# Kernel tuning notes

Hardware: AMD Instinct MI355X
Metric: run time of the kernel (lower is better)

## Reference

```python
import jax, jax.numpy as jnp
from jax import lax
import numpy as np

KSIZE = 5  # kernel_size from init
CHANNEL = 256

def _gaussian_kernel2d(sigma, ksize):
    # matches torch: exp(-i^2/(2*sigma^2)) outer product, normalized to sum 1
    n = ksize // 2
    r = jnp.arange(-n, n + 1, dtype=jnp.float32)
    g = jnp.exp(-(r ** 2) / (2.0 * sigma ** 2))
    k2d = g[:, None] * g[None, :]
    return k2d / k2d.sum()

def setup_inputs() -> dict:
    key = jax.random.key(0)
    k1, k2 = jax.random.split(key)
    x = jax.random.normal(k1, (16, CHANNEL, 64, 64), dtype=jnp.float32)
    # sigma is the module's learned scalar; keep away from 0 for a well-defined kernel
    sigma = jax.random.uniform(k2, (1,), dtype=jnp.float32, minval=0.5, maxval=1.5)
    return {"x": x, "sigma": sigma}

def reference(x, sigma):
    # The torch module writes a channel-diagonal weight into a dense Conv2d;
    # mathematically this is a depthwise conv with the same 2D Gaussian per channel.
    C = x.shape[1]
    k2d = _gaussian_kernel2d(sigma[0], KSIZE)
    w = jnp.broadcast_to(k2d[None, None, :, :], (C, 1, KSIZE, KSIZE))  # OIHW, groups=C
    pad = KSIZE // 2
    return lax.conv_general_dilated(
        x, w,
        window_strides=(1, 1),
        padding=[(pad, pad), (pad, pad)],
        dimension_numbers=("NCHW", "OIHW", "NCHW"),
        feature_group_count=C,
    )
```

## Files before the change

### kernel.cpp

```cpp
#include <hip/hip_runtime.h>
#include <math.h>


constexpr int Hh   = 64;
constexpr int Ww   = 64;
constexpr int KS   = 5;
constexpr int PADc = 2;
constexpr int TH   = Hh + 2 * PADc;
constexpr int IN_STR = 72;

__global__ __launch_bounds__(256, 6) void gauss5(const float* __restrict__ x,
                                                 const float* __restrict__ sigma,
                                                 float* __restrict__ out) {
    __shared__ float sIn[TH * IN_STR];

    const int t = threadIdx.x;
    const size_t plane = blockIdx.x;
    const float* __restrict__ xp = x + plane * (size_t)(Hh * Ww);
    float* __restrict__ op = out + plane * (size_t)(Hh * Ww);

    const float sg = sigma[0];
    const float c2 = -1.0f / (2.0f * sg * sg);
    float g[KS];
    float gsum = 0.0f;
#pragma unroll
    for (int i = 0; i < KS; ++i) {
        float d = (float)(i - PADc);
        g[i] = expf(d * d * c2);
        gsum += g[i];
    }
    const float ginv = 1.0f / gsum;
#pragma unroll
    for (int i = 0; i < KS; ++i) g[i] *= ginv;

    for (int i = t; i < 528; i += 256) {
        if (i < 272) {
            int rr  = i / 68;
            int cc  = i - rr * 68;
            int row = (rr < 2) ? rr : (rr + 64);
            sIn[row * IN_STR + cc] = 0.0f;
        } else {
            int j   = i - 272;
            int row = 2 + (j >> 2);
            int k   = j & 3;
            int col = (k < 2) ? k : (k + 64);
            sIn[row * IN_STR + col] = 0.0f;
        }
    }

    const float4* __restrict__ x4 = (const float4*)xp;
#pragma unroll
    for (int k = 0; k < 4; ++k) {
        int idx = t + k * 256;
        int r   = idx >> 4;
        int c   = (idx & 15) << 2;
        float4 v = x4[idx];
        float* dst = &sIn[(r + PADc) * IN_STR + c + PADc];
        dst[0] = v.x; dst[1] = v.y; dst[2] = v.z; dst[3] = v.w;
    }
    __syncthreads();

    const int c4 = t & 15;
    const int r0 = (t >> 4) << 2;

    float4 h[8];
#pragma unroll
    for (int i = 0; i < 8; ++i) {
        const float* src = &sIn[(r0 + i) * IN_STR + (c4 << 2)];
        float4 a = *(const float4*)(src);
        float4 b = *(const float4*)(src + 4);
        h[i].x = g[0]*a.x + g[1]*a.y + g[2]*a.z + g[3]*a.w + g[4]*b.x;
        h[i].y = g[0]*a.y + g[1]*a.z + g[2]*a.w + g[3]*b.x + g[4]*b.y;
        h[i].z = g[0]*a.z + g[1]*a.w + g[2]*b.x + g[3]*b.y + g[4]*b.z;
        h[i].w = g[0]*a.w + g[1]*b.x + g[2]*b.y + g[3]*b.z + g[4]*b.w;
    }

    float4* __restrict__ o4 = (float4*)op;
#pragma unroll
    for (int i = 0; i < 4; ++i) {
        float4 acc;
        acc.x = g[0]*h[i].x; acc.y = g[0]*h[i].y;
        acc.z = g[0]*h[i].z; acc.w = g[0]*h[i].w;
#pragma unroll
        for (int j = 1; j < KS; ++j) {
            acc.x += g[j] * h[i+j].x;
            acc.y += g[j] * h[i+j].y;
            acc.z += g[j] * h[i+j].z;
            acc.w += g[j] * h[i+j].w;
        }
        o4[(r0 + i) * 16 + c4] = acc;
    }
}

extern "C" void kernel_launch(void* const* d_in, const int* in_sizes, int n_in,
                              void* d_out, int out_size, void* d_ws, size_t ws_size,
                              hipStream_t stream) {
    const float* x     = (const float*)d_in[0];
    const float* sigma = (const float*)d_in[1];
    float* out         = (float*)d_out;
    const int planes = in_sizes[0] / (Hh * Ww);
    gauss5<<<planes, 256, 0, stream>>>(x, sigma, out);
}
```

Before: 118.7 us.

## Process four planes per block with double-buffered LDS and register prefetch

```diff
diff --git a/kernel.cpp b/kernel.cpp
--- a/kernel.cpp
+++ b/kernel.cpp
@@ -8,16 +8,15 @@
 constexpr int PADc = 2;
 constexpr int TH   = Hh + 2 * PADc;
 constexpr int IN_STR = 72;
+constexpr int PPB  = 4;
 
-__global__ __launch_bounds__(256, 6) void gauss5(const float* __restrict__ x,
+__global__ __launch_bounds__(256, 4) void gauss5(const float* __restrict__ x,
                                                  const float* __restrict__ sigma,
                                                  float* __restrict__ out) {
-    __shared__ float sIn[TH * IN_STR];
+    __shared__ alignas(16) float sIn[2][TH * IN_STR];
 
     const int t = threadIdx.x;
-    const size_t plane = blockIdx.x;
-    const float* __restrict__ xp = x + plane * (size_t)(Hh * Ww);
-    float* __restrict__ op = out + plane * (size_t)(Hh * Ww);
+    const size_t plane0 = (size_t)blockIdx.x * PPB;
 
     const float sg = sigma[0];
     const float c2 = -1.0f / (2.0f * sg * sg);
@@ -34,61 +33,89 @@
     for (int i = 0; i < KS; ++i) g[i] *= ginv;
 
     for (int i = t; i < 528; i += 256) {
+        int row, col;
         if (i < 272) {
-            int rr  = i / 68;
-            int cc  = i - rr * 68;
-            int row = (rr < 2) ? rr : (rr + 64);
-            sIn[row * IN_STR + cc] = 0.0f;
+            int rr = i / 68;
+            col = i - rr * 68;
+            row = (rr < 2) ? rr : (rr + 64);
         } else {
-            int j   = i - 272;
-            int row = 2 + (j >> 2);
-            int k   = j & 3;
-            int col = (k < 2) ? k : (k + 64);
-            sIn[row * IN_STR + col] = 0.0f;
+            int j = i - 272;
+            row = 2 + (j >> 2);
+            int k = j & 3;
+            col = (k < 2) ? k : (k + 64);
         }
+        sIn[0][row * IN_STR + col] = 0.0f;
+        sIn[1][row * IN_STR + col] = 0.0f;
     }
-
-    const float4* __restrict__ x4 = (const float4*)xp;
-#pragma unroll
-    for (int k = 0; k < 4; ++k) {
-        int idx = t + k * 256;
-        int r   = idx >> 4;
-        int c   = (idx & 15) << 2;
-        float4 v = x4[idx];
-        float* dst = &sIn[(r + PADc) * IN_STR + c + PADc];
-        dst[0] = v.x; dst[1] = v.y; dst[2] = v.z; dst[3] = v.w;
-    }
-    __syncthreads();
 
     const int c4 = t & 15;
     const int r0 = (t >> 4) << 2;
 
-    float4 h[8];
+    float4 v[4];
+    {
+        const float4* __restrict__ x4 = (const float4*)(x + plane0 * (Hh * Ww));
 #pragma unroll
-    for (int i = 0; i < 8; ++i) {
-        const float* src = &sIn[(r0 + i) * IN_STR + (c4 << 2)];
-        float4 a = *(const float4*)(src);
-        float4 b = *(const float4*)(src + 4);
-        h[i].x = g[0]*a.x + g[1]*a.y + g[2]*a.z + g[3]*a.w + g[4]*b.x;
-        h[i].y = g[0]*a.y + g[1]*a.z + g[2]*a.w + g[3]*b.x + g[4]*b.y;
-        h[i].z = g[0]*a.z + g[1]*a.w + g[2]*b.x + g[3]*b.y + g[4]*b.z;
-        h[i].w = g[0]*a.w + g[1]*b.x + g[2]*b.y + g[3]*b.z + g[4]*b.w;
+        for (int k = 0; k < 4; ++k) v[k] = x4[t + k * 256];
+#pragma unroll
+        for (int k = 0; k < 4; ++k) {
+            int idx = t + k * 256;
+            int r   = idx >> 4;
+            int c   = (idx & 15) << 2;
+            float* dst = &sIn[0][(r + PADc) * IN_STR + c + PADc];
+            dst[0] = v[k].x; dst[1] = v[k].y; dst[2] = v[k].z; dst[3] = v[k].w;
+        }
     }
+    __syncthreads();
 
-    float4* __restrict__ o4 = (float4*)op;
+    for (int p = 0; p < PPB; ++p) {
+        if (p + 1 < PPB) {
+            const float4* __restrict__ xn =
+                (const float4*)(x + (plane0 + p + 1) * (Hh * Ww));
 #pragma unroll
-    for (int i = 0; i < 4; ++i) {
-        float4 acc;
-        acc.x = g[0]*h[i].x; acc.y = g[0]*h[i].y;
-        acc.z = g[0]*h[i].z; acc.w = g[0]*h[i].w;
+            for (int k = 0; k < 4; ++k) v[k] = xn[t + k * 256];
+        }
+
+        const float* __restrict__ buf = sIn[p & 1];
+        float4 h[8];
 #pragma unroll
-        for (int j = 1; j < KS; ++j) {
-            acc.x += g[j] * h[i+j].x;
-            acc.y += g[j] * h[i+j].y;
-            acc.z += g[j] * h[i+j].z;
-            acc.w += g[j] * h[i+j].w;
+        for (int i = 0; i < 8; ++i) {
+            const float* src = &buf[(r0 + i) * IN_STR + (c4 << 2)];
+            float4 a = *(const float4*)(src);
+            float4 b = *(const float4*)(src + 4);
+            h[i].x = g[0]*a.x + g[1]*a.y + g[2]*a.z + g[3]*a.w + g[4]*b.x;
+            h[i].y = g[0]*a.y + g[1]*a.z + g[2]*a.w + g[3]*b.x + g[4]*b.y;
+            h[i].z = g[0]*a.z + g[1]*a.w + g[2]*b.x + g[3]*b.y + g[4]*b.z;
+            h[i].w = g[0]*a.w + g[1]*b.x + g[2]*b.y + g[3]*b.z + g[4]*b.w;
         }
-        o4[(r0 + i) * 16 + c4] = acc;
+
+        float4* __restrict__ o4 = (float4*)(out + (plane0 + p) * (Hh * Ww));
+#pragma unroll
+        for (int i = 0; i < 4; ++i) {
+            float4 acc;
+            acc.x = g[0]*h[i].x; acc.y = g[0]*h[i].y;
+            acc.z = g[0]*h[i].z; acc.w = g[0]*h[i].w;
+#pragma unroll
+            for (int j = 1; j < KS; ++j) {
+                acc.x += g[j] * h[i+j].x;
+                acc.y += g[j] * h[i+j].y;
+                acc.z += g[j] * h[i+j].z;
+                acc.w += g[j] * h[i+j].w;
+            }
+            o4[(r0 + i) * 16 + c4] = acc;
+        }
+
+        if (p + 1 < PPB) {
+            float* __restrict__ nbuf = sIn[(p + 1) & 1];
+#pragma unroll
+            for (int k = 0; k < 4; ++k) {
+                int idx = t + k * 256;
+                int r   = idx >> 4;
+                int c   = (idx & 15) << 2;
+                float* dst = &nbuf[(r + PADc) * IN_STR + c + PADc];
+                dst[0] = v[k].x; dst[1] = v[k].y; dst[2] = v[k].z; dst[3] = v[k].w;
+            }
+            __syncthreads();
+        }
     }
 }
 
@@ -99,5 +126,5 @@
     const float* sigma = (const float*)d_in[1];
     float* out         = (float*)d_out;
     const int planes = in_sizes[0] / (Hh * Ww);
-    gauss5<<<planes, 256, 0, stream>>>(x, sigma, out);
+    gauss5<<<planes / PPB, 256, 0, stream>>>(x, sigma, out);
 }
```

Result: faster. 112.2 us (-5.4%).
